# Kernel optimization log

Measured on AMD Instinct MI355X. Metric: run time of the kernel, lower is better.

The kernel has to match this reference:

```python
import jax, jax.numpy as jnp
import numpy as np

H = 5  # hidden size (hardcoded in the torch module)


def setup_inputs() -> dict:
    key = jax.random.key(0)
    ks = jax.random.split(key, 9)
    N, T = 32768, 600
    s = 1.0 / np.sqrt(H)  # torch LSTM/Linear init scale (uniform bound), use as stddev
    return {
        "x": jax.random.normal(ks[0], (N, T), dtype=jnp.float32),
        "w_ih": jax.random.normal(ks[1], (4 * H, 1), dtype=jnp.float32) * s,
        "w_hh": jax.random.normal(ks[2], (4 * H, H), dtype=jnp.float32) * s,
        "b_ih": jax.random.normal(ks[3], (4 * H,), dtype=jnp.float32) * s,
        "b_hh": jax.random.normal(ks[4], (4 * H,), dtype=jnp.float32) * s,
        "fc_w": jax.random.normal(ks[5], (15, H), dtype=jnp.float32) * s,
        "fc_b": jax.random.normal(ks[6], (15,), dtype=jnp.float32) * s,
        "out_w": jax.random.normal(ks[7], (1, 15), dtype=jnp.float32) * (1.0 / np.sqrt(15)),
        "out_b": jax.random.normal(ks[8], (1,), dtype=jnp.float32) * (1.0 / np.sqrt(15)),
    }


def reference(x, w_ih, w_hh, b_ih, b_hh, fc_w, fc_b, out_w, out_b):
    # x: (N, T) -> unsqueeze to feature dim of 1 is implicit (input_size=1).
    N = x.shape[0]
    b = b_ih + b_hh  # (4H,)
    w_ih_vec = w_ih[:, 0]  # (4H,) since input_size == 1

    def step(carry, x_t):
        h, c = carry  # (N, H) each
        # gates: (N, 4H); PyTorch gate order: i, f, g, o
        gates = x_t[:, None] * w_ih_vec + h @ w_hh.T + b
        i = jax.nn.sigmoid(gates[:, 0 * H:1 * H])
        f = jax.nn.sigmoid(gates[:, 1 * H:2 * H])
        g = jnp.tanh(gates[:, 2 * H:3 * H])
        o = jax.nn.sigmoid(gates[:, 3 * H:4 * H])
        c = f * c + i * g
        h = o * jnp.tanh(c)
        return (h, c), None

    h0 = jnp.zeros((N, H), dtype=x.dtype)
    c0 = jnp.zeros((N, H), dtype=x.dtype)
    (h_T, _), _ = jax.lax.scan(step, (h0, c0), x.T)  # scan over time: xs (T, N)
    # Head: only the last timestep's hidden state is used.
    hid = h_T @ fc_w.T + fc_b          # (N, 15)
    out = hid @ out_w.T + out_b        # (N, 1)
    return jax.nn.sigmoid(out)
```

## Files before the change

### kernel.cpp

```cpp
#include <hip/hip_runtime.h>
#include <math.h>


#define LOG2E 1.44269504088896340736f

typedef float v2f __attribute__((ext_vector_type(2)));

constexpr int T_ = 600;
constexpr int SEQ_PER_BLOCK = 32;
constexpr int TTILE = 64;
constexpr int NTILES = (T_ + TTILE - 1) / TTILE;
constexpr int LDS_STRIDE = 68;
constexpr int XBUF = SEQ_PER_BLOCK * LDS_STRIDE;

__device__ __forceinline__ float fast_rcp(float v)  { return __builtin_amdgcn_rcpf(v); }
__device__ __forceinline__ float fast_exp2(float v) { return __builtin_amdgcn_exp2f(v); }

template <int CTRL>
__device__ __forceinline__ float dpp_q(float v) {
    const int x = __float_as_int(v);
    return __int_as_float(__builtin_amdgcn_update_dpp(x, x, CTRL, 0xF, 0xF, false));
}

__global__ __launch_bounds__(64, 1) void lstm_kernel(
    const float* __restrict__ x,
    const float* __restrict__ w_ih,
    const float* __restrict__ w_hh,
    const float* __restrict__ b_ih,
    const float* __restrict__ b_hh,
    const float* __restrict__ fc_w,
    const float* __restrict__ fc_b,
    const float* __restrict__ out_w,
    const float* __restrict__ out_b,
    float* __restrict__ out)
{
    __shared__ float xs[2 * XBUF];

    const int lane = threadIdx.x;
    const int s    = lane >> 1;
    const int half = lane & 1;
    const int seq  = blockIdx.x * SEQ_PER_BLOCK + s;

    const int rloT[2][5] = {{0, 1, 2, 5, 6}, {3, 4, 7, 8, 9}};
    const int rhiT[2][5] = {{10, 11, 12, 15, 16}, {13, 14, 17, 18, 19}};
    const int gtT [2][5] = {{1, 1, 1, 0, 0}, {1, 1, 0, 0, 0}};

    v2f wih2[5], bb2[5], whh2[5][5], A2[5], B2[5];
#pragma unroll
    for (int p = 0; p < 5; ++p) {
        const int rlo = rloT[half][p], rhi = rhiT[half][p];
        const int gt  = gtT[half][p];
        const float sl = -LOG2E;
        const float sh = gt ? (-2.0f * LOG2E) : (-LOG2E);
        wih2[p] = (v2f){ w_ih[rlo] * sl, w_ih[rhi] * sh };
        bb2[p]  = (v2f){ (b_ih[rlo] + b_hh[rlo]) * sl,
                         (b_ih[rhi] + b_hh[rhi]) * sh };
#pragma unroll
        for (int k = 0; k < 5; ++k)
            whh2[p][k] = (v2f){ w_hh[rlo * 5 + k] * sl, w_hh[rhi * 5 + k] * sh };
        A2[p] = (v2f){ 1.0f, gt ? (-4.0f * LOG2E) : 1.0f };
        B2[p] = (v2f){ 0.0f, gt ? ( 2.0f * LOG2E) : 0.0f };
    }

    float H[5] = {0.f, 0.f, 0.f, 0.f, 0.f};
    float cA = 0.f, cB = 0.f, cC = 0.f;

    const float* xblk = x + (size_t)(blockIdx.x * SEQ_PER_BLOCK) * T_;

    auto step = [&](float xt) {
        const v2f x2 = (v2f){ xt, xt };
        v2f g2[5];
#pragma unroll
        for (int p = 0; p < 5; ++p) g2[p] = x2 * wih2[p] + bb2[p];
#pragma unroll
        for (int k = 0; k < 5; ++k) {
            const v2f h2 = (v2f){ H[k], H[k] };
#pragma unroll
            for (int p = 0; p < 5; ++p) g2[p] += h2 * whh2[p][k];
        }
        v2f act2[5];
#pragma unroll
        for (int p = 0; p < 5; ++p) {
            v2f d2;
            d2.x = 1.0f + fast_exp2(g2[p].x);
            d2.y = 1.0f + fast_exp2(g2[p].y);
            const float rp = fast_rcp(d2.x * d2.y);
            const v2f r2 = (v2f){ rp * d2.y, rp * d2.x };
            act2[p] = r2 * A2[p] + B2[p];
        }
        const float PA = act2[0].x * act2[0].y;
        const float PB = act2[1].x * act2[1].y;
        const float P2 = dpp_q<0xA0>(act2[2].x * act2[2].y);
        const float f2 = dpp_q<0xF5>(act2[2].x);
        const float o2 = dpp_q<0xF5>(act2[2].y);
        cA = fmaf(act2[3].x, cA, PA);
        cB = fmaf(act2[4].x, cB, PB);
        cC = fmaf(f2, cC, P2);
        const float dA = 1.0f + fast_exp2(cA);
        const float dB = 1.0f + fast_exp2(cB);
        const float dC = 1.0f + fast_exp2(cC);
        const float q  = fast_rcp(dA * dB);
        const float tA = fmaf(q * dB, 2.0f, -1.0f);
        const float tB = fmaf(q * dA, 2.0f, -1.0f);
        const float tC = fmaf(fast_rcp(dC), 2.0f, -1.0f);
        const float hA = act2[3].y * tA;
        const float hB = act2[4].y * tB;
        const float hC = o2 * tC;
        H[0] = dpp_q<0xA0>(hA);
        H[1] = dpp_q<0xA0>(hB);
        H[2] = hC;
        H[3] = dpp_q<0xF5>(hA);
        H[4] = dpp_q<0xF5>(hB);
    };

    const int rrow = lane >> 4;
    const int ccol = (lane & 15) << 2;

#pragma unroll
    for (int it = 0; it < 8; ++it) {
        const int r = it * 4 + rrow;
        const float4 v = *(const float4*)(xblk + (size_t)r * T_ + ccol);
        *(float4*)&xs[r * LDS_STRIDE + ccol] = v;
    }
    __syncthreads();

    for (int tile = 0; tile < NTILES; ++tile) {
        float4 pf[8];
        const int tn  = tile + 1;
        const int t0n = tn * TTILE;
        if (tn < NTILES) {
#pragma unroll
            for (int it = 0; it < 8; ++it) {
                const int r = it * 4 + rrow;
                if (t0n + ccol < T_)
                    pf[it] = *(const float4*)(xblk + (size_t)r * T_ + (t0n + ccol));
            }
        }
        const int t0i  = tile * TTILE;
        const int steps = min(TTILE, T_ - t0i);
        const float* xr = &xs[(tile & 1) * XBUF + s * LDS_STRIDE];
        for (int tt = 0; tt < steps; tt += 4) {
            const float4 xv4 = *(const float4*)&xr[tt];
            step(xv4.x);
            step(xv4.y);
            step(xv4.z);
            step(xv4.w);
        }
        if (tn < NTILES) {
#pragma unroll
            for (int it = 0; it < 8; ++it) {
                const int r = it * 4 + rrow;
                if (t0n + ccol < T_)
                    *(float4*)&xs[(tn & 1) * XBUF + r * LDS_STRIDE + ccol] = pf[it];
            }
            __syncthreads();
        }
    }

    if (half == 0) {
        float acc = out_b[0];
#pragma unroll
        for (int j = 0; j < 15; ++j) {
            float hid = fc_b[j];
#pragma unroll
            for (int k = 0; k < 5; ++k) hid = fmaf(H[k], fc_w[j * 5 + k], hid);
            acc = fmaf(hid, out_w[j], acc);
        }
        out[seq] = fast_rcp(1.0f + fast_exp2(-acc * LOG2E));
    }
}

extern "C" void kernel_launch(void* const* d_in, const int* in_sizes, int n_in,
                              void* d_out, int out_size, void* d_ws, size_t ws_size,
                              hipStream_t stream) {
    const float* x    = (const float*)d_in[0];
    const float* w_ih = (const float*)d_in[1];
    const float* w_hh = (const float*)d_in[2];
    const float* b_ih = (const float*)d_in[3];
    const float* b_hh = (const float*)d_in[4];
    const float* fc_w = (const float*)d_in[5];
    const float* fc_b = (const float*)d_in[6];
    const float* out_w = (const float*)d_in[7];
    const float* out_b = (const float*)d_in[8];
    float* out = (float*)d_out;

    const int N = in_sizes[0] / T_;
    const int grid = N / SEQ_PER_BLOCK;
    hipLaunchKernelGGL(lstm_kernel, dim3(grid), dim3(64), 0, stream,
                       x, w_ih, w_hh, b_ih, b_hh, fc_w, fc_b, out_w, out_b, out);
}
```

Baseline: 260.8 us.

## Drop double-buffered prefetch and per-gate affine registers to cut VGPR pressure

Replaces the double-buffered LDS tile with a register prefetch by a single buffer that is loaded synchronously before each tile. It also removes the per-gate A2/B2 constant vectors and applies the tanh affine transform through a lane-dependent conditional FMA. Both changes lower register and LDS use, which could raise occupancy or free registers for the recurrence. The cost is that global load latency is now exposed at every tile boundary instead of overlapping with compute.

```diff
diff --git a/kernel.cpp b/kernel.cpp
--- a/kernel.cpp
+++ b/kernel.cpp
@@ -9,9 +9,7 @@
 constexpr int T_ = 600;
 constexpr int SEQ_PER_BLOCK = 32;
 constexpr int TTILE = 64;
-constexpr int NTILES = (T_ + TTILE - 1) / TTILE;
 constexpr int LDS_STRIDE = 68;
-constexpr int XBUF = SEQ_PER_BLOCK * LDS_STRIDE;
 
 __device__ __forceinline__ float fast_rcp(float v)  { return __builtin_amdgcn_rcpf(v); }
 __device__ __forceinline__ float fast_exp2(float v) { return __builtin_amdgcn_exp2f(v); }
@@ -34,7 +32,7 @@
     const float* __restrict__ out_b,
     float* __restrict__ out)
 {
-    __shared__ float xs[2 * XBUF];
+    __shared__ float xs[SEQ_PER_BLOCK * LDS_STRIDE];
 
     const int lane = threadIdx.x;
     const int s    = lane >> 1;
@@ -45,22 +43,20 @@
     const int rhiT[2][5] = {{10, 11, 12, 15, 16}, {13, 14, 17, 18, 19}};
     const int gtT [2][5] = {{1, 1, 1, 0, 0}, {1, 1, 0, 0, 0}};
 
-    v2f wih2[5], bb2[5], whh2[5][5], A2[5], B2[5];
+    v2f wih2[5], bb2[5], whh2[5][5];
 #pragma unroll
     for (int p = 0; p < 5; ++p) {
         const int rlo = rloT[half][p], rhi = rhiT[half][p];
-        const int gt  = gtT[half][p];
         const float sl = -LOG2E;
-        const float sh = gt ? (-2.0f * LOG2E) : (-LOG2E);
+        const float sh = gtT[half][p] ? (-2.0f * LOG2E) : (-LOG2E);
         wih2[p] = (v2f){ w_ih[rlo] * sl, w_ih[rhi] * sh };
         bb2[p]  = (v2f){ (b_ih[rlo] + b_hh[rlo]) * sl,
                          (b_ih[rhi] + b_hh[rhi]) * sh };
 #pragma unroll
         for (int k = 0; k < 5; ++k)
             whh2[p][k] = (v2f){ w_hh[rlo * 5 + k] * sl, w_hh[rhi * 5 + k] * sh };
-        A2[p] = (v2f){ 1.0f, gt ? (-4.0f * LOG2E) : 1.0f };
-        B2[p] = (v2f){ 0.0f, gt ? ( 2.0f * LOG2E) : 0.0f };
     }
+    const int ng = half ? 2 : 3;
 
     float H[5] = {0.f, 0.f, 0.f, 0.f, 0.f};
     float cA = 0.f, cB = 0.f, cC = 0.f;
@@ -81,13 +77,16 @@
         v2f act2[5];
 #pragma unroll
         for (int p = 0; p < 5; ++p) {
-            v2f d2;
-            d2.x = 1.0f + fast_exp2(g2[p].x);
-            d2.y = 1.0f + fast_exp2(g2[p].y);
-            const float rp = fast_rcp(d2.x * d2.y);
-            const v2f r2 = (v2f){ rp * d2.y, rp * d2.x };
-            act2[p] = r2 * A2[p] + B2[p];
+            const float dx = 1.0f + fast_exp2(g2[p].x);
+            const float dy = 1.0f + fast_exp2(g2[p].y);
+            const float rp = fast_rcp(dx * dy);
+            act2[p].x = rp * dy;
+            act2[p].y = rp * dx;
         }
+#pragma unroll
+        for (int p = 0; p < 3; ++p)
+            if (p < ng)
+                act2[p].y = fmaf(act2[p].y, -4.0f * LOG2E, 2.0f * LOG2E);
         const float PA = act2[0].x * act2[0].y;
         const float PB = act2[1].x * act2[1].y;
         const float P2 = dpp_q<0xA0>(act2[2].x * act2[2].y);
@@ -105,10 +104,9 @@
         const float tC = fmaf(fast_rcp(dC), 2.0f, -1.0f);
         const float hA = act2[3].y * tA;
         const float hB = act2[4].y * tB;
-        const float hC = o2 * tC;
         H[0] = dpp_q<0xA0>(hA);
         H[1] = dpp_q<0xA0>(hB);
-        H[2] = hC;
+        H[2] = o2 * tC;
         H[3] = dpp_q<0xF5>(hA);
         H[4] = dpp_q<0xF5>(hB);
     };
@@ -116,44 +114,26 @@
     const int rrow = lane >> 4;
     const int ccol = (lane & 15) << 2;
 
+    for (int t0i = 0; t0i < T_; t0i += TTILE) {
+        __syncthreads();
 #pragma unroll
-    for (int it = 0; it < 8; ++it) {
-        const int r = it * 4 + rrow;
-        const float4 v = *(const float4*)(xblk + (size_t)r * T_ + ccol);
-        *(float4*)&xs[r * LDS_STRIDE + ccol] = v;
-    }
-    __syncthreads();
-
-    for (int tile = 0; tile < NTILES; ++tile) {
-        float4 pf[8];
-        const int tn  = tile + 1;
-        const int t0n = tn * TTILE;
-        if (tn < NTILES) {
-#pragma unroll
-            for (int it = 0; it < 8; ++it) {
-                const int r = it * 4 + rrow;
-                if (t0n + ccol < T_)
-                    pf[it] = *(const float4*)(xblk + (size_t)r * T_ + (t0n + ccol));
+        for (int it = 0; it < 8; ++it) {
+            const int r = it * 4 + rrow;
+            if (t0i + ccol < T_) {
+                const float4 v = *(const float4*)(xblk + (size_t)r * T_ + (t0i + ccol));
+                *(float4*)&xs[r * LDS_STRIDE + ccol] = v;
             }
         }
-        const int t0i  = tile * TTILE;
+        __syncthreads();
+
         const int steps = min(TTILE, T_ - t0i);
-        const float* xr = &xs[(tile & 1) * XBUF + s * LDS_STRIDE];
+        const float* xr = &xs[s * LDS_STRIDE];
         for (int tt = 0; tt < steps; tt += 4) {
             const float4 xv4 = *(const float4*)&xr[tt];
             step(xv4.x);
             step(xv4.y);
             step(xv4.z);
             step(xv4.w);
-        }
-        if (tn < NTILES) {
-#pragma unroll
-            for (int it = 0; it < 8; ++it) {
-                const int r = it * 4 + rrow;
-                if (t0n + ccol < T_)
-                    *(float4*)&xs[(tn & 1) * XBUF + r * LDS_STRIDE + ccol] = pf[it];
-            }
-            __syncthreads();
         }
     }
 
```

Result: no change. 258.3 us (-1.0%).
